# Kernel optimization log

Hardware: AMD Instinct MI355X
Metric: run time of the kernel (lower is better)

The kernel has to match this reference:

```python
import jax, jax.numpy as jnp
import numpy as np

NB, NA, NC, NH, NW = 32, 5, 80, 64, 64
MAXT = 50
STRIDE = 32.0
ANCHORS_PX = [42.3, 55.4, 102.2, 128.3, 161.8, 259.2, 303.1, 154.9, 359.6, 320.2]
NOOBJECT_SCALE, OBJECT_SCALE = 1.0, 5.0
COORD_SCALE, CLASS_SCALE = 1.0, 1.0
SIL_THRESH = 0.6


def _iou_center(ax, ay, aw, ah, bx, by, bw, bh):
    # IoU for boxes in (cx, cy, w, h) form; zero when no overlap (matches bbox_ious x1y1x2y2=False)
    iw = jnp.minimum(ax + aw * 0.5, bx + bw * 0.5) - jnp.maximum(ax - aw * 0.5, bx - bw * 0.5)
    ih = jnp.minimum(ay + ah * 0.5, by + bh * 0.5) - jnp.maximum(ay - ah * 0.5, by - bh * 0.5)
    inter = jnp.maximum(iw, 0.0) * jnp.maximum(ih, 0.0)
    union = aw * ah + bw * bh - inter
    return inter / union


def _region_loss(output, target):
    sg = jax.lax.stop_gradient
    anchors = jnp.array(ANCHORS_PX, jnp.float32).reshape(NA, 2) / STRIDE  # anchors scaled by stride
    out = output.reshape(NB, NA, 5 + NC, NH, NW)
    x = jax.nn.sigmoid(out[:, :, 0])
    y = jax.nn.sigmoid(out[:, :, 1])
    w = out[:, :, 2]
    h = out[:, :, 3]
    conf = jax.nn.sigmoid(out[:, :, 4])
    cls_logits = jnp.transpose(out[:, :, 5:], (0, 1, 3, 4, 2))  # [B,A,H,W,C]

    grid_x = jnp.arange(NW, dtype=jnp.float32)[None, None, None, :]
    grid_y = jnp.arange(NH, dtype=jnp.float32)[None, None, :, None]
    aw = anchors[:, 0][None, :, None, None]
    ah = anchors[:, 1][None, :, None, None]
    # decoded pred boxes are detached in the torch code (built from .data)
    px = sg(x) + grid_x
    py = sg(y) + grid_y
    pw = jnp.exp(sg(w)) * aw
    ph = jnp.exp(sg(h)) * ah

    tgt = sg(target).reshape(NB, MAXT, 5)  # [cls, x, y, w, h] per target, normalized
    gcls = tgt[:, :, 0]
    gx = tgt[:, :, 1] * NW
    gy = tgt[:, :, 2] * NH
    gw = tgt[:, :, 3] * NW
    gh = tgt[:, :, 4] * NH
    # loop breaks at first target with x == 0 -> cumulative validity
    valid = jnp.cumprod((tgt[:, :, 1] != 0).astype(jnp.float32), axis=1) > 0  # [B,T]

    # --- conf mask silencing: max IoU of each pred box against all GT boxes ---
    ious = _iou_center(px[..., None], py[..., None], pw[..., None], ph[..., None],
                       gx[:, None, None, None, :], gy[:, None, None, None, :],
                       gw[:, None, None, None, :], gh[:, None, None, None, :])  # [B,A,H,W,T]
    ious = jnp.where(valid[:, None, None, None, :], ious, 0.0)
    cur_ious = jnp.max(ious, axis=-1)
    conf_mask0 = jnp.where(cur_ious > SIL_THRESH, 0.0, NOOBJECT_SCALE)

    # --- best anchor per GT: wh-only IoU at origin (anchor_step == 2) ---
    inter = jnp.minimum(gw[..., None], anchors[None, None, :, 0]) * \
            jnp.minimum(gh[..., None], anchors[None, None, :, 1])  # [B,T,A]
    union = gw[..., None] * gh[..., None] + anchors[None, None, :, 0] * anchors[None, None, :, 1] - inter
    best_n = jnp.argmax(inter / union, axis=-1)

    gi = jnp.clip(gx.astype(jnp.int32), 0, NW - 1)
    gj = jnp.clip(gy.astype(jnp.int32), 0, NH - 1)
    bidx = jnp.arange(NB, dtype=jnp.int32)[:, None]
    aw_b = anchors[best_n, 0]
    ah_b = anchors[best_n, 1]

    pb_x = px[bidx, best_n, gj, gi]
    pb_y = py[bidx, best_n, gj, gi]
    pb_w = pw[bidx, best_n, gj, gi]
    pb_h = ph[bidx, best_n, gj, gi]
    t_iou = _iou_center(gx, gy, gw, gh, pb_x, pb_y, pb_w, pb_h)  # [B,T]

    N = NB * NA * NH * NW
    flat = ((bidx * NA + best_n) * NH + gj) * NW + gi
    flat = jnp.where(valid, flat, N).reshape(-1)  # invalid targets scattered to dummy slot

    def scat(base, vals):
        padded = jnp.concatenate([base.reshape(-1), jnp.zeros((1,), base.dtype)])
        return padded.at[flat].set(vals.reshape(-1))[:N].reshape(NB, NA, NH, NW)

    ones_t = jnp.ones_like(gx)
    # seen=0 < 12800 -> coord_mask = 1 everywhere, tx=ty=0.5, tw=th=0 as base
    coord_mask = scat(jnp.ones((NB, NA, NH, NW), jnp.float32), ones_t)
    cls_mask = scat(jnp.zeros((NB, NA, NH, NW), jnp.float32), ones_t)
    conf_mask = scat(conf_mask0, jnp.full_like(gx, OBJECT_SCALE))
    txg = scat(jnp.full((NB, NA, NH, NW), 0.5, jnp.float32), gx - gi.astype(jnp.float32))
    tyg = scat(jnp.full((NB, NA, NH, NW), 0.5, jnp.float32), gy - gj.astype(jnp.float32))
    twg = scat(jnp.zeros((NB, NA, NH, NW), jnp.float32), jnp.log(gw / aw_b))
    thg = scat(jnp.zeros((NB, NA, NH, NW), jnp.float32), jnp.log(gh / ah_b))
    tconf = scat(jnp.zeros((NB, NA, NH, NW), jnp.float32), t_iou)
    tcls = scat(jnp.zeros((NB, NA, NH, NW), jnp.float32), gcls)

    conf_m = jnp.sqrt(conf_mask)
    loss_x = COORD_SCALE * jnp.sum((x * coord_mask - txg * coord_mask) ** 2) / 2.0
    loss_y = COORD_SCALE * jnp.sum((y * coord_mask - tyg * coord_mask) ** 2) / 2.0
    loss_w = COORD_SCALE * jnp.sum((w * coord_mask - twg * coord_mask) ** 2) / 2.0
    loss_h = COORD_SCALE * jnp.sum((h * coord_mask - thg * coord_mask) ** 2) / 2.0
    loss_conf = jnp.sum((conf * conf_m - tconf * conf_m) ** 2) / 2.0
    # CrossEntropy over cells where cls_mask == 1 (sum reduction)
    logZ = jax.nn.logsumexp(cls_logits, axis=-1)
    picked = jnp.take_along_axis(cls_logits, tcls.astype(jnp.int32)[..., None], axis=-1)[..., 0]
    loss_cls = CLASS_SCALE * jnp.sum((logZ - picked) * cls_mask)
    return loss_x + loss_y + loss_w + loss_h + loss_conf + loss_cls


def setup_inputs() -> dict:
    key = jax.random.key(0)
    k1, k2, k3, k4 = jax.random.split(key, 4)
    output = jax.random.normal(k1, (NB, NA * (5 + NC), NH, NW), jnp.float32) * 0.5
    cls_ids = jax.random.randint(k2, (NB, MAXT), 0, NC).astype(jnp.float32)
    xy = jax.random.uniform(k3, (NB, MAXT, 2), jnp.float32, minval=0.05, maxval=0.95)
    wh = jax.random.uniform(k4, (NB, MAXT, 2), jnp.float32, minval=0.05, maxval=0.4)
    target = jnp.concatenate([cls_ids[..., None], xy, wh], axis=-1).reshape(NB, MAXT * 5)
    return {"output": output, "target": target}


def reference(output, target):
    return _region_loss(output, target)
```

## Files before the change

kernel.cpp:

```cpp
#include <hip/hip_runtime.h>

#define NB 32
#define NA 5
#define NC 80
#define NH 64
#define NW 64
#define MAXT 50
#define CH 85
#define HW (NH*NW)
#define NBLK (NB*NA*HW/256)
#define BPB (NA*HW/256)

__constant__ float c_aw[NA] = {42.3f/32.0f, 102.2f/32.0f, 161.8f/32.0f, 303.1f/32.0f, 359.6f/32.0f};
__constant__ float c_ah[NA] = {55.4f/32.0f, 128.3f/32.0f, 259.2f/32.0f, 154.9f/32.0f, 320.2f/32.0f};

__device__ __forceinline__ float sigm(float x) {
    return __builtin_amdgcn_rcpf(1.0f + __expf(-x));
}

__global__ __launch_bounds__(256) void fused_kernel(const float* __restrict__ out,
                                                    const float* __restrict__ tgt,
                                                    float* __restrict__ W) {
    const int blk = blockIdx.x;
    const int tid = threadIdx.x;
    const int b   = blk / BPB;
    const int r   = blk - b*BPB;
    const int a   = r >> 4;
    const int ji  = ((r & 15) << 8) + tid;
    const int i   = ji & (NW-1);
    const int j   = ji >> 6;

    __shared__ float sxl[MAXT], sxh[MAXT], syl[MAXT], syh[MAXT], sga[MAXT];
    __shared__ float sgx[MAXT], sgy[MAXT], sgw[MAXT], sgh[MAXT], sgc[MAXT];
    __shared__ int   s_id[MAXT];
    __shared__ int   s_eid[MAXT];
    __shared__ float s_tx[MAXT], s_ty[MAXT], s_tw[MAXT], s_th[MAXT], s_ti[MAXT];
    __shared__ int   s_ec[MAXT];
    __shared__ int   s_nv;
    __shared__ float red[4];

    if (tid < 64) {
        bool iszero = true;
        if (tid < MAXT) {
            const float* p = tgt + (b*MAXT + tid)*5;
            const float gcls = p[0];
            const float rx = p[1];
            iszero = (rx == 0.0f);
            const float gx = rx   * (float)NW;
            const float gy = p[2] * (float)NH;
            const float gw = p[3] * (float)NW;
            const float gh = p[4] * (float)NH;
            sxl[tid] = gx - 0.5f*gw; sxh[tid] = gx + 0.5f*gw;
            syl[tid] = gy - 0.5f*gh; syh[tid] = gy + 0.5f*gh;
            sga[tid] = 0.375f*gw*gh;
            sgx[tid] = gx; sgy[tid] = gy; sgw[tid] = gw; sgh[tid] = gh; sgc[tid] = gcls;
        }
        unsigned long long mz = __ballot(iszero);
        if (tid == 0) s_nv = __ffsll(mz) - 1;
    }
    __syncthreads();
    const int nv = s_nv;

    const size_t base = (size_t)((b*NA + a)*CH)*HW + ji;
    const float ox = out[base];
    const float oy = out[base + HW];
    const float ow = out[base + 2*HW];
    const float oh = out[base + 3*HW];
    const float oc = out[base + 4*HW];

    const float sx = sigm(ox);
    const float sy = sigm(oy);
    const float sc = sigm(oc);
    const float pw = __expf(ow) * c_aw[a];
    const float ph = __expf(oh) * c_ah[a];
    const float px = sx + (float)i;
    const float py = sy + (float)j;
    const float pxl = px - 0.5f*pw, pxh = px + 0.5f*pw;
    const float pyl = py - 0.5f*ph, pyh = py + 0.5f*ph;
    const float pa375 = 0.375f * pw * ph;

    float m = -1.0f;
    for (int tt = 0; tt < nv; tt++) {
        float iw = fminf(pxh, sxh[tt]) - fmaxf(pxl, sxl[tt]);
        float ih = fminf(pyh, syh[tt]) - fmaxf(pyl, syl[tt]);
        float inter = fmaxf(iw, 0.f) * fmaxf(ih, 0.f);
        m = fmaxf(m, inter - sga[tt]);
    }
    const bool over = m > pa375;

    const float dx = sx - 0.5f, dy = sy - 0.5f;
    float v = dx*dx + dy*dy + ow*ow + oh*oh;
    if (!over) v += sc*sc;
    v *= 0.5f;

    for (int off = 32; off > 0; off >>= 1) v += __shfl_down(v, off);
    if ((tid & 63) == 0) red[tid >> 6] = v;
    __syncthreads();
    float bsum = (tid == 0) ? (red[0] + red[1] + red[2] + red[3]) : 0.0f;

    if (r == 0) {
        if (tid < 64 && tid < nv) {
            const float gx = sgx[tid], gy = sgy[tid], gw = sgw[tid], gh = sgh[tid];
            const float garea = gw * gh;
            float best = -1.0f; int bn = 0;
            #pragma unroll
            for (int n = 0; n < NA; n++) {
                float inter = fminf(gw, c_aw[n]) * fminf(gh, c_ah[n]);
                float uni = garea + c_aw[n]*c_ah[n] - inter;
                float rr = inter / uni;
                if (rr > best) { best = rr; bn = n; }
            }
            int gi = (int)gx; gi = gi < 0 ? 0 : (gi > NW-1 ? NW-1 : gi);
            int gj = (int)gy; gj = gj < 0 ? 0 : (gj > NH-1 ? NH-1 : gj);
            const float awb = c_aw[bn], ahb = c_ah[bn];

            const size_t gbase = (size_t)((b*NA + bn)*CH)*HW + gj*NW + gi;
            const float o0 = out[gbase];
            const float o1 = out[gbase + HW];
            const float o2 = out[gbase + 2*HW];
            const float o3 = out[gbase + 3*HW];
            const float ppx = sigm(o0) + (float)gi;
            const float ppy = sigm(o1) + (float)gj;
            const float ppw = __expf(o2) * awb;
            const float pph = __expf(o3) * ahb;
            const float iw = fminf(gx + 0.5f*gw, ppx + 0.5f*ppw) - fmaxf(gx - 0.5f*gw, ppx - 0.5f*ppw);
            const float ih = fminf(gy + 0.5f*gh, ppy + 0.5f*pph) - fmaxf(gy - 0.5f*gh, ppy - 0.5f*pph);
            const float inter = fmaxf(iw, 0.f) * fmaxf(ih, 0.f);
            const float tiou = inter / (garea + ppw*pph - inter);

            s_id[tid] = (bn*NH + gj)*NW + gi;
            s_tx[tid] = gx - (float)gi;
            s_ty[tid] = gy - (float)gj;
            s_tw[tid] = __logf(gw / awb);
            s_th[tid] = __logf(gh / ahb);
            s_ti[tid] = tiou;
            s_ec[tid] = (int)sgc[tid];
        }
        __syncthreads();
        if (tid < nv) {
            const int myid = s_id[tid];
            bool keep = true;
            for (int u = tid + 1; u < nv; u++)
                if (s_id[u] == myid) { keep = false; break; }
            s_eid[tid] = keep ? myid : -1;
        }
        __syncthreads();

        float acc = 0.0f;
        const int e = tid >> 2;
        const int q = tid & 3;
        if (e < nv) {
            const int id = s_eid[e];
            if (id >= 0) {
                const int ea  = id >> 12;
                const int eji = id & (HW-1);
                const int eii = eji & (NW-1);
                const int ejj = eji >> 6;
                const size_t eb = (size_t)((b*NA + ea)*CH)*HW + eji;
                const float cox = out[eb];
                const float coy = out[eb + HW];
                const float cow = out[eb + 2*HW];
                const float coh = out[eb + 3*HW];
                const float coc = out[eb + 4*HW];
                const float csx = sigm(cox), csy = sigm(coy), csc = sigm(coc);
                const float cpw = __expf(cow) * c_aw[ea];
                const float cph = __expf(coh) * c_ah[ea];
                const float cpx = csx + (float)eii, cpy = csy + (float)ejj;
                const float cxl = cpx - 0.5f*cpw, cxh = cpx + 0.5f*cpw;
                const float cyl = cpy - 0.5f*cph, cyh = cpy + 0.5f*cph;
                const float cpa = 0.375f * cpw * cph;

                float mm = -1.0f;
                for (int u = q; u < nv; u += 4) {
                    float iw = fminf(cxh, sxh[u]) - fmaxf(cxl, sxl[u]);
                    float ih = fminf(cyh, syh[u]) - fmaxf(cyl, syl[u]);
                    float inter = fmaxf(iw, 0.f) * fmaxf(ih, 0.f);
                    mm = fmaxf(mm, inter - sga[u]);
                }
                mm = fmaxf(mm, __shfl_xor(mm, 1));
                mm = fmaxf(mm, __shfl_xor(mm, 2));

                const float* lg = out + eb + 5*HW;
                float rch[20];
                #pragma unroll
                for (int k = 0; k < 20; k++) rch[k] = lg[(size_t)(q + 4*k)*HW];
                float mx = rch[0];
                #pragma unroll
                for (int k = 1; k < 20; k++) mx = fmaxf(mx, rch[k]);
                mx = fmaxf(mx, __shfl_xor(mx, 1));
                mx = fmaxf(mx, __shfl_xor(mx, 2));
                float s = 0.0f;
                #pragma unroll
                for (int k = 0; k < 20; k++) s += __expf(rch[k] - mx);
                s += __shfl_xor(s, 1);
                s += __shfl_xor(s, 2);

                if (q == 0) {
                    const float tx = s_tx[e], ty = s_ty[e], tw = s_tw[e], th = s_th[e], ti = s_ti[e];
                    const int cls = s_ec[e];
                    const float dxn = csx - tx, dxo = csx - 0.5f;
                    const float dyn = csy - ty, dyo = csy - 0.5f;
                    const float dwn = cow - tw, dhn = coh - th;
                    float d = dxn*dxn - dxo*dxo + dyn*dyn - dyo*dyo
                            + dwn*dwn - cow*cow + dhn*dhn - coh*coh;
                    float dc = 5.f*(csc - ti)*(csc - ti);
                    if (!(mm > cpa)) dc -= csc*csc;
                    d += dc;
                    acc += 0.5f * d;
                    acc += mx + __logf(s) - lg[(size_t)cls*HW];
                }
            }
        }
        for (int off = 32; off > 0; off >>= 1) acc += __shfl_down(acc, off);
        if ((tid & 63) == 0) red[tid >> 6] = acc;
        __syncthreads();
        if (tid == 0) bsum += red[0] + red[1] + red[2] + red[3];
    }

    if (tid == 0) W[blk] = bsum;
}

__global__ __launch_bounds__(256) void fin_kernel(const float* __restrict__ W,
                                                  float* __restrict__ res) {
    float s = 0.0f;
    for (int k = threadIdx.x; k < NBLK; k += 256) s += W[k];
    for (int off = 32; off > 0; off >>= 1) s += __shfl_down(s, off);
    __shared__ float red[4];
    if ((threadIdx.x & 63) == 0) red[threadIdx.x >> 6] = s;
    __syncthreads();
    if (threadIdx.x == 0) res[0] = red[0] + red[1] + red[2] + red[3];
}

extern "C" void kernel_launch(void* const* d_in, const int* in_sizes, int n_in,
                              void* d_out, int out_size, void* d_ws, size_t ws_size,
                              hipStream_t stream) {
    const float* out = (const float*)d_in[0];
    const float* tgt = (const float*)d_in[1];
    float* W = (float*)d_ws;
    float* res = (float*)d_out;
    hipLaunchKernelGGL(fused_kernel, dim3(NBLK), dim3(256), 0, stream, out, tgt, W);
    hipLaunchKernelGGL(fin_kernel, dim3(1), dim3(256), 0, stream, W, res);
}
```

Baseline: 300.8 us.

## Process two cells per thread and skip non-overlapping targets with wave-uniform test

Halves the block count so each thread evaluates two grid cells (rows j and j+4), amortising the target loop across both. Each wave computes nv itself with a ballot instead of waiting on a shared-memory setup barrier, and reads target boxes directly from global memory. It also checks vertical overlap first and skips the x-side IoU work when no lane in the wave overlaps. This trades fewer blocks and possible extra global/scalar loads per target for less redundant work and one fewer barrier.

```diff
diff --git a/kernel.cpp b/kernel.cpp
--- a/kernel.cpp
+++ b/kernel.cpp
@@ -8,8 +8,8 @@
 #define MAXT 50
 #define CH 85
 #define HW (NH*NW)
-#define NBLK (NB*NA*HW/256)
-#define BPB (NA*HW/256)
+#define BPB 40
+#define NBLK (NB*BPB)
 
 __constant__ float c_aw[NA] = {42.3f/32.0f, 102.2f/32.0f, 161.8f/32.0f, 303.1f/32.0f, 359.6f/32.0f};
 __constant__ float c_ah[NA] = {55.4f/32.0f, 128.3f/32.0f, 259.2f/32.0f, 154.9f/32.0f, 320.2f/32.0f};
@@ -25,82 +25,91 @@
     const int tid = threadIdx.x;
     const int b   = blk / BPB;
     const int r   = blk - b*BPB;
-    const int a   = r >> 4;
-    const int ji  = ((r & 15) << 8) + tid;
-    const int i   = ji & (NW-1);
-    const int j   = ji >> 6;
+    const int a   = r >> 3;
+    const int ji0 = ((r & 7) << 9) + tid;
+    const int i0  = ji0 & (NW-1);
+    const int j0  = ji0 >> 6;
+
+    const int lane = tid & 63;
+    bool isz = true;
+    if (lane < MAXT) isz = (tgt[(b*MAXT + lane)*5 + 1] == 0.0f);
+    const int nv = __ffsll(__ballot(isz)) - 1;
+
+    const size_t base0 = (size_t)((b*NA + a)*CH)*HW + ji0;
+    const float ox0 = out[base0],        ox1 = out[base0+256];
+    const float oy0 = out[base0+HW],     oy1 = out[base0+HW+256];
+    const float ow0 = out[base0+2*HW],   ow1 = out[base0+2*HW+256];
+    const float oh0 = out[base0+3*HW],   oh1 = out[base0+3*HW+256];
+    const float oc0 = out[base0+4*HW],   oc1 = out[base0+4*HW+256];
+
+    const float aw = c_aw[a], ah = c_ah[a];
+    const float sx0 = sigm(ox0), sy0 = sigm(oy0), sc0 = sigm(oc0);
+    const float sx1 = sigm(ox1), sy1 = sigm(oy1), sc1 = sigm(oc1);
+    const float pw0 = __expf(ow0)*aw, ph0 = __expf(oh0)*ah;
+    const float pw1 = __expf(ow1)*aw, ph1 = __expf(oh1)*ah;
+    const float px0 = sx0 + (float)i0, py0 = sy0 + (float)j0;
+    const float px1 = sx1 + (float)i0, py1 = sy1 + (float)(j0+4);
+    const float pxl0 = px0 - 0.5f*pw0, pxh0 = px0 + 0.5f*pw0;
+    const float pyl0 = py0 - 0.5f*ph0, pyh0 = py0 + 0.5f*ph0;
+    const float pxl1 = px1 - 0.5f*pw1, pxh1 = px1 + 0.5f*pw1;
+    const float pyl1 = py1 - 0.5f*ph1, pyh1 = py1 + 0.5f*ph1;
+    const float pa0 = 0.375f*pw0*ph0;
+    const float pa1 = 0.375f*pw1*ph1;
+
+    float m0 = -1.0f, m1 = -1.0f;
+    const float* __restrict__ tb = tgt + (size_t)b*MAXT*5;
+    for (int tt = 0; tt < nv; tt++) {
+        const int t5 = tt*5;
+        const float gy = tb[t5+2] * (float)NH;
+        const float gh = tb[t5+4] * (float)NH;
+        const float tyl = gy - 0.5f*gh;
+        const float tyh = gy + 0.5f*gh;
+        const float ih0 = fminf(pyh0, tyh) - fmaxf(pyl0, tyl);
+        const float ih1 = fminf(pyh1, tyh) - fmaxf(pyl1, tyl);
+        if (__any((ih0 > 0.0f) || (ih1 > 0.0f))) {
+            const float gx = tb[t5+1] * (float)NW;
+            const float gw = tb[t5+3] * (float)NW;
+            const float txl = gx - 0.5f*gw;
+            const float txh = gx + 0.5f*gw;
+            const float ga  = 0.375f*(gw*gh);
+            const float iw0 = fminf(pxh0, txh) - fmaxf(pxl0, txl);
+            const float iw1 = fminf(pxh1, txh) - fmaxf(pxl1, txl);
+            const float in0 = fmaxf(iw0, 0.f) * fmaxf(ih0, 0.f);
+            const float in1 = fmaxf(iw1, 0.f) * fmaxf(ih1, 0.f);
+            m0 = fmaxf(m0, in0 - ga);
+            m1 = fmaxf(m1, in1 - ga);
+        }
+    }
+
+    const float dx0 = sx0 - 0.5f, dy0 = sy0 - 0.5f;
+    float v0 = dx0*dx0 + dy0*dy0 + ow0*ow0 + oh0*oh0;
+    if (!(m0 > pa0)) v0 += sc0*sc0;
+    const float dx1 = sx1 - 0.5f, dy1 = sy1 - 0.5f;
+    float v1 = dx1*dx1 + dy1*dy1 + ow1*ow1 + oh1*oh1;
+    if (!(m1 > pa1)) v1 += sc1*sc1;
+    float v = (v0 + v1) * 0.5f;
+
+    __shared__ float red[4];
+    for (int off = 32; off > 0; off >>= 1) v += __shfl_down(v, off);
+    if ((tid & 63) == 0) red[tid >> 6] = v;
+    __syncthreads();
+    float bsum = (tid == 0) ? (red[0] + red[1] + red[2] + red[3]) : 0.0f;
 
     __shared__ float sxl[MAXT], sxh[MAXT], syl[MAXT], syh[MAXT], sga[MAXT];
-    __shared__ float sgx[MAXT], sgy[MAXT], sgw[MAXT], sgh[MAXT], sgc[MAXT];
-    __shared__ int   s_id[MAXT];
-    __shared__ int   s_eid[MAXT];
+    __shared__ int   s_id[MAXT], s_eid[MAXT], s_ec[MAXT];
     __shared__ float s_tx[MAXT], s_ty[MAXT], s_tw[MAXT], s_th[MAXT], s_ti[MAXT];
-    __shared__ int   s_ec[MAXT];
-    __shared__ int   s_nv;
-    __shared__ float red[4];
-
-    if (tid < 64) {
-        bool iszero = true;
-        if (tid < MAXT) {
+    if (r == 0) {
+        if (tid < 64 && tid < nv) {
             const float* p = tgt + (b*MAXT + tid)*5;
             const float gcls = p[0];
-            const float rx = p[1];
-            iszero = (rx == 0.0f);
-            const float gx = rx   * (float)NW;
+            const float gx = p[1] * (float)NW;
             const float gy = p[2] * (float)NH;
             const float gw = p[3] * (float)NW;
             const float gh = p[4] * (float)NH;
             sxl[tid] = gx - 0.5f*gw; sxh[tid] = gx + 0.5f*gw;
             syl[tid] = gy - 0.5f*gh; syh[tid] = gy + 0.5f*gh;
             sga[tid] = 0.375f*gw*gh;
-            sgx[tid] = gx; sgy[tid] = gy; sgw[tid] = gw; sgh[tid] = gh; sgc[tid] = gcls;
-        }
-        unsigned long long mz = __ballot(iszero);
-        if (tid == 0) s_nv = __ffsll(mz) - 1;
-    }
-    __syncthreads();
-    const int nv = s_nv;
-
-    const size_t base = (size_t)((b*NA + a)*CH)*HW + ji;
-    const float ox = out[base];
-    const float oy = out[base + HW];
-    const float ow = out[base + 2*HW];
-    const float oh = out[base + 3*HW];
-    const float oc = out[base + 4*HW];
-
-    const float sx = sigm(ox);
-    const float sy = sigm(oy);
-    const float sc = sigm(oc);
-    const float pw = __expf(ow) * c_aw[a];
-    const float ph = __expf(oh) * c_ah[a];
-    const float px = sx + (float)i;
-    const float py = sy + (float)j;
-    const float pxl = px - 0.5f*pw, pxh = px + 0.5f*pw;
-    const float pyl = py - 0.5f*ph, pyh = py + 0.5f*ph;
-    const float pa375 = 0.375f * pw * ph;
-
-    float m = -1.0f;
-    for (int tt = 0; tt < nv; tt++) {
-        float iw = fminf(pxh, sxh[tt]) - fmaxf(pxl, sxl[tt]);
-        float ih = fminf(pyh, syh[tt]) - fmaxf(pyl, syl[tt]);
-        float inter = fmaxf(iw, 0.f) * fmaxf(ih, 0.f);
-        m = fmaxf(m, inter - sga[tt]);
-    }
-    const bool over = m > pa375;
-
-    const float dx = sx - 0.5f, dy = sy - 0.5f;
-    float v = dx*dx + dy*dy + ow*ow + oh*oh;
-    if (!over) v += sc*sc;
-    v *= 0.5f;
-
-    for (int off = 32; off > 0; off >>= 1) v += __shfl_down(v, off);
-    if ((tid & 63) == 0) red[tid >> 6] = v;
-    __syncthreads();
-    float bsum = (tid == 0) ? (red[0] + red[1] + red[2] + red[3]) : 0.0f;
-
-    if (r == 0) {
-        if (tid < 64 && tid < nv) {
-            const float gx = sgx[tid], gy = sgy[tid], gw = sgw[tid], gh = sgh[tid];
+
             const float garea = gw * gh;
             float best = -1.0f; int bn = 0;
             #pragma unroll
@@ -134,7 +143,7 @@
             s_tw[tid] = __logf(gw / awb);
             s_th[tid] = __logf(gh / ahb);
             s_ti[tid] = tiou;
-            s_ec[tid] = (int)sgc[tid];
+            s_ec[tid] = (int)gcls;
         }
         __syncthreads();
         if (tid < nv) {
```

New measurement: 280.3 us. 6.8% less time.
